# Optimization experiments

Hardware: AMD Instinct MI355X
Metric: run time of the kernel (lower is better)

The kernel has to match this reference:

```python
import jax, jax.numpy as jnp
import numpy as np

DIM = 192
NUM_HEADS = 6
KSZ = 7
MLP_RATIO = 4.0
LEVELS = 8
EPS = 1e-5


def layernorm(x, w, b):
    mu = jnp.mean(x, axis=-1, keepdims=True)
    var = jnp.mean(jnp.square(x - mu), axis=-1, keepdims=True)
    return (x - mu) * jax.lax.rsqrt(var + EPS) * w + b


def na2d(x, qkv_w, qkv_b, proj_w, proj_b, rpb):
    # Neighborhood attention 2D with relative position bias (NATTEN semantics:
    # window of KSZ x KSZ keys per query, clamped to stay inside the image).
    B, H, W, C = x.shape
    nh, hd = NUM_HEADS, C // NUM_HEADS
    scale = hd ** -0.5
    qkv = (x @ qkv_w.T + qkv_b).reshape(B, H, W, 3, nh, hd)
    q = qkv[..., 0, :, :] * scale  # [B,H,W,nh,hd]
    k = qkv[..., 1, :, :]
    v = qkv[..., 2, :, :]

    si = jnp.clip(jnp.arange(H) - KSZ // 2, 0, H - KSZ)
    idx_i = si[:, None] + jnp.arange(KSZ)  # [H,KSZ] row indices of each window
    sj = jnp.clip(jnp.arange(W) - KSZ // 2, 0, W - KSZ)
    idx_j = sj[:, None] + jnp.arange(KSZ)  # [W,KSZ]

    def gather_win(t):  # [B,H,W,nh,hd] -> [B,H,KSZ,W,KSZ,nh,hd]
        t = jnp.take(t, idx_i.reshape(-1), axis=1).reshape(B, H, KSZ, W, nh, hd)
        t = jnp.take(t, idx_j.reshape(-1), axis=3).reshape(B, H, KSZ, W, KSZ, nh, hd)
        return t

    kw = gather_win(k)
    vw = gather_win(v)

    # scores over the KSZ x KSZ neighborhood
    scores = jnp.einsum('bxynd,bxiyjnd->bxynij', q, kw)  # [B,H,W,nh,KSZ,KSZ]

    # relative position bias: rpb is [nh, 2K-1, 2K-1]
    rel_i = idx_i - jnp.arange(H)[:, None] + (KSZ - 1)  # [H,KSZ] in [0,2K-2]
    rel_j = idx_j - jnp.arange(W)[:, None] + (KSZ - 1)  # [W,KSZ]
    bias = rpb[:, rel_i][:, :, :, rel_j]  # [nh,H,KSZ,W,KSZ]
    scores = scores + bias.transpose(1, 3, 0, 2, 4)[None]

    attn = jax.nn.softmax(scores.reshape(B, H, W, nh, KSZ * KSZ), axis=-1)
    attn = attn.reshape(B, H, W, nh, KSZ, KSZ)
    out = jnp.einsum('bxynij,bxiyjnd->bxynd', attn, vw).reshape(B, H, W, C)
    return out @ proj_w.T + proj_b


def setup_inputs() -> dict:
    key = jax.random.key(0)
    ks = jax.random.split(key, 8)
    C = DIM
    hidden = int(C * MLP_RATIO)
    init = lambda k, shape: (jax.random.normal(k, shape, dtype=jnp.float32) * 0.02)
    return {
        'x': jax.random.normal(ks[0], (1, 128, 128, C), dtype=jnp.float32),
        'qkv_w': init(ks[1], (3 * C, C)),
        'qkv_b': jnp.zeros((3 * C,), jnp.float32),
        'proj_w': init(ks[2], (C, C)),
        'proj_b': jnp.zeros((C,), jnp.float32),
        'rpb': init(ks[3], (NUM_HEADS, 2 * KSZ - 1, 2 * KSZ - 1)),
        'ln1_w': jnp.ones((C,), jnp.float32),
        'ln1_b': jnp.zeros((C,), jnp.float32),
        'ln2_w': jnp.ones((C,), jnp.float32),
        'ln2_b': jnp.zeros((C,), jnp.float32),
        'fc1_w': init(ks[4], (hidden, C)),
        'fc1_b': jnp.zeros((hidden,), jnp.float32),
        'fc2_w': init(ks[5], (C, hidden)),
        'fc2_b': jnp.zeros((C,), jnp.float32),
        'gamma1': jnp.ones((LEVELS, C), jnp.float32),
        'gamma2': jnp.ones((LEVELS, C), jnp.float32),
        'quality': 4,
    }


def reference(x, qkv_w, qkv_b, proj_w, proj_b, rpb, ln1_w, ln1_b, ln2_w, ln2_b,
              fc1_w, fc1_b, fc2_w, fc2_b, gamma1, gamma2, quality):
    # eval-mode quality gating; quality is an integer so l = quality % 1 == 0
    s = int(quality) - 1
    g1 = jnp.abs(gamma1[s])
    g2 = jnp.abs(gamma2[s])

    shortcut = x
    h = layernorm(x, ln1_w, ln1_b)
    a = na2d(h, qkv_w, qkv_b, proj_w, proj_b, rpb)
    x = shortcut + g1 * a
    h2 = layernorm(x, ln2_w, ln2_b)
    m = jax.nn.gelu(h2 @ fc1_w.T + fc1_b, approximate=False) @ fc2_w.T + fc2_b
    x = x + g2 * m
    return x
```

## Files before the change

kernel.cpp:

```cpp
#include <hip/hip_runtime.h>
#include <hip/hip_bf16.h>
#include <math.h>

#define DIM 192
#define NHD 6
#define HD 32
#define KSZ 7
#define HID 768
#define IMH 128
#define IMW 128
#define NPIX (IMH*IMW)
#define WIN 14
#define KPAD 40

typedef __attribute__((ext_vector_type(8))) short short8;
typedef __attribute__((ext_vector_type(4))) float f32x4;

__global__ __launch_bounds__(256) void cvt_w(
    const float* __restrict__ qw, const float* __restrict__ pw,
    const float* __restrict__ f1, const float* __restrict__ f2,
    __hip_bfloat16* dq, __hip_bfloat16* dp, __hip_bfloat16* df1, __hip_bfloat16* df2)
{
    int blk = blockIdx.x, t = threadIdx.x;
    const float* s; __hip_bfloat16* d; int base;
    if (blk < 108)      { s = qw; d = dq;  base = blk * 1024; }
    else if (blk < 144) { s = pw; d = dp;  base = (blk - 108) * 1024; }
    else if (blk < 288) { s = f1; d = df1; base = (blk - 144) * 1024; }
    else                { s = f2; d = df2; base = (blk - 288) * 1024; }
    int idx = base + t * 4;
    float4 v4 = *(const float4*)(s + idx);
    union { ushort4 u; __hip_bfloat16 h[4]; } o;
    o.h[0] = __float2bfloat16(v4.x); o.h[1] = __float2bfloat16(v4.y);
    o.h[2] = __float2bfloat16(v4.z); o.h[3] = __float2bfloat16(v4.w);
    *(ushort4*)&d[idx] = o.u;
}

__device__ __forceinline__ void gl_lds16(const void* g, void* l) {
    __builtin_amdgcn_global_load_lds(
        (const __attribute__((address_space(1))) void*)g,
        (__attribute__((address_space(3))) void*)l, 16, 0, 0);
}

__device__ __forceinline__ short8 cvt8(float4 a, float4 b) {
    union { short8 v; __hip_bfloat16 h[8]; } u;
    u.h[0] = __float2bfloat16(a.x); u.h[1] = __float2bfloat16(a.y);
    u.h[2] = __float2bfloat16(a.z); u.h[3] = __float2bfloat16(a.w);
    u.h[4] = __float2bfloat16(b.x); u.h[5] = __float2bfloat16(b.y);
    u.h[6] = __float2bfloat16(b.z); u.h[7] = __float2bfloat16(b.w);
    return u.v;
}

__global__ __launch_bounds__(256, 2) void qkv_ln_gemm(
    const float* __restrict__ x, const float* __restrict__ lnw, const float* __restrict__ lnb,
    const __hip_bfloat16* __restrict__ W, const float* __restrict__ bias,
    float* __restrict__ qb, __hip_bfloat16* __restrict__ kb, __hip_bfloat16* __restrict__ vb)
{
    __shared__ __hip_bfloat16 As[32 * 192];
    __shared__ __hip_bfloat16 Ws2[2][64 * 192];
    int tid = threadIdx.x;
    int wave = tid >> 6, lane = tid & 63;
    int q = lane >> 4, col = lane & 15;
    int wm = (wave >> 1) * 16, wn = (wave & 1) * 32;
    int m0 = blockIdx.x * 32;

    auto stageW = [&](int ch, int buf) {
        #pragma unroll
        for (int i = 0; i < 6; i++) {
            int c = i * 256 + tid;
            int r = c / 24, kc = c - r * 24;
            gl_lds16(W + (size_t)(ch * 64 + r) * DIM + ((kc ^ (r & 7)) * 8),
                     (char*)&Ws2[buf][0] + (i * 256 + wave * 64) * 16);
        }
    };

    stageW(0, 0);

    {
        int row = tid >> 3, sub = tid & 7;
        const float4* xr = (const float4*)(x + (size_t)(m0 + row) * DIM + sub * 24);
        float4 xa[6];
        float s = 0.f;
        #pragma unroll
        for (int i = 0; i < 6; i++) {
            xa[i] = xr[i];
            s += xa[i].x + xa[i].y + xa[i].z + xa[i].w;
        }
        s += __shfl_xor(s, 1); s += __shfl_xor(s, 2); s += __shfl_xor(s, 4);
        float mu = s * (1.0f / DIM);
        float qs = 0.f;
        #pragma unroll
        for (int i = 0; i < 6; i++) {
            float a = xa[i].x - mu, b = xa[i].y - mu, c = xa[i].z - mu, d = xa[i].w - mu;
            qs += a * a + b * b + c * c + d * d;
        }
        qs += __shfl_xor(qs, 1); qs += __shfl_xor(qs, 2); qs += __shfl_xor(qs, 4);
        float rstd = rsqrtf(qs * (1.0f / DIM) + 1e-5f);
        const float4* wv = (const float4*)(lnw + sub * 24);
        const float4* bv = (const float4*)(lnb + sub * 24);
        #pragma unroll
        for (int j = 0; j < 3; j++) {
            float4 v0 = xa[j * 2], v1 = xa[j * 2 + 1];
            float4 w0 = wv[j * 2], w1 = wv[j * 2 + 1];
            float4 b0 = bv[j * 2], b1 = bv[j * 2 + 1];
            float4 o0, o1;
            o0.x = (v0.x - mu) * rstd * w0.x + b0.x;
            o0.y = (v0.y - mu) * rstd * w0.y + b0.y;
            o0.z = (v0.z - mu) * rstd * w0.z + b0.z;
            o0.w = (v0.w - mu) * rstd * w0.w + b0.w;
            o1.x = (v1.x - mu) * rstd * w1.x + b1.x;
            o1.y = (v1.y - mu) * rstd * w1.y + b1.y;
            o1.z = (v1.z - mu) * rstd * w1.z + b1.z;
            o1.w = (v1.w - mu) * rstd * w1.w + b1.w;
            int oct = sub * 3 + j;
            *(short8*)&As[row * 192 + ((oct ^ (row & 7)) * 8)] = cvt8(o0, o1);
        }
    }
    asm volatile("s_waitcnt lgkmcnt(0)" ::: "memory");
    __builtin_amdgcn_s_barrier();

    short8 af[6];
    {
        int rA = wm + col;
        #pragma unroll
        for (int ks = 0; ks < 6; ks++)
            af[ks] = *(const short8*)&As[rA * 192 + (((ks * 4 + q) ^ (rA & 7)) * 8)];
    }

    for (int ch = 0; ch < 9; ch++) {
        if (ch < 8) {
            stageW(ch + 1, (ch + 1) & 1);
            asm volatile("s_waitcnt vmcnt(6)" ::: "memory");
        } else {
            asm volatile("s_waitcnt vmcnt(0)" ::: "memory");
        }
        __builtin_amdgcn_s_barrier();
        const __hip_bfloat16* wsb = &Ws2[ch & 1][0];
        f32x4 acc[2] = {};
        #pragma unroll
        for (int ks = 0; ks < 6; ks++) {
            #pragma unroll
            for (int ni = 0; ni < 2; ni++) {
                int rB = wn + ni * 16 + col;
                short8 bf = *(const short8*)&wsb[rB * 192 + (((ks * 4 + q) ^ (rB & 7)) * 8)];
                acc[ni] = __builtin_amdgcn_mfma_f32_16x16x32_bf16(af[ks], bf, acc[ni], 0, 0, 0);
            }
        }
        #pragma unroll
        for (int ni = 0; ni < 2; ni++) {
            int n = ch * 64 + wn + ni * 16 + col;
            float bi = bias[n];
            int h18 = n >> 5;
            int sel = h18 / 6;
            int head = h18 - sel * 6;
            #pragma unroll
            for (int r4 = 0; r4 < 4; r4++) {
                int m = m0 + wm + q * 4 + r4;
                float v = acc[ni][r4] + bi;
                size_t idx = ((size_t)head * NPIX + m) * 32 + (n & 31);
                if (sel == 0)      qb[idx] = v * 0.17677669529663687f;
                else if (sel == 1) kb[idx] = __float2bfloat16(v);
                else               vb[idx] = __float2bfloat16(v);
            }
        }
        __builtin_amdgcn_s_barrier();
    }
}

__global__ __launch_bounds__(512, 2) void tail_fused(
    const __hip_bfloat16* __restrict__ A, const __hip_bfloat16* __restrict__ Wp,
    const float* __restrict__ pb, const float* __restrict__ resid,
    const float* __restrict__ gamma1, const float* __restrict__ ln2w, const float* __restrict__ ln2b,
    const __hip_bfloat16* __restrict__ W1, const float* __restrict__ b1,
    const __hip_bfloat16* __restrict__ W2, const float* __restrict__ b2,
    const float* __restrict__ gamma2, const int* __restrict__ quality,
    float* __restrict__ outf)
{
    __shared__ __hip_bfloat16 arena[64 * 768];
    __shared__ __hip_bfloat16 Wsb[2][64 * 192];
    __shared__ float lnred[2][64][2];
    __hip_bfloat16* Bsp = arena;
    __hip_bfloat16* Hs  = arena + 192 * 192;

    int tid = threadIdx.x;
    int wave = tid >> 6, lane = tid & 63;
    int q = lane >> 4, col = lane & 15;
    int wm = (wave >> 1) * 16, wh = wave & 1;
    int m0 = blockIdx.x * 64;

    const __hip_bfloat16* Ab = A + (size_t)m0 * DIM;
    #pragma unroll
    for (int i = 0; i < 3; i++) {
        int c = i * 512 + tid;
        int r = c / 24, kc = c - r * 24;
        gl_lds16(Ab + r * DIM + (kc ^ (r & 7)) * 8, (char*)Hs + (i * 512 + wave * 64) * 16);
    }
    #pragma unroll
    for (int i = 0; i < 9; i++) {
        int c = i * 512 + tid;
        int r = c / 24, kc = c - r * 24;
        gl_lds16(Wp + (size_t)r * DIM + (kc ^ (r & 7)) * 8, (char*)Bsp + (i * 512 + wave * 64) * 16);
    }
    __syncthreads();

    f32x4 acc[6] = {};
    #pragma unroll
    for (int ks = 0; ks < 6; ks++) {
        int rA = wm + col;
        short8 af = *(const short8*)&Hs[rA * DIM + (((ks * 4 + q) ^ (rA & 7)) * 8)];
        #pragma unroll
        for (int f = 0; f < 6; f++) {
            int rB = wh * 96 + f * 16 + col;
            short8 bf = *(const short8*)&Bsp[rB * DIM + (((ks * 4 + q) ^ (rB & 7)) * 8)];
            acc[f] = __builtin_amdgcn_mfma_f32_16x16x32_bf16(af, bf, acc[f], 0, 0, 0);
        }
    }

    int s = quality[0] - 1;
    float v[6][4];
    float sm[4] = {}, sq[4] = {};
    #pragma unroll
    for (int f = 0; f < 6; f++) {
        int n = wh * 96 + f * 16 + col;
        float bi = pb[n];
        float g = fabsf(gamma1[s * DIM + n]);
        #pragma unroll
        for (int r = 0; r < 4; r++) {
            int m = m0 + wm + q * 4 + r;
            v[f][r] = resid[(size_t)m * DIM + n] + g * (acc[f][r] + bi);
            sm[r] += v[f][r]; sq[r] += v[f][r] * v[f][r];
        }
    }
    #pragma unroll
    for (int off = 1; off <= 8; off <<= 1)
        #pragma unroll
        for (int r = 0; r < 4; r++) {
            sm[r] += __shfl_xor(sm[r], off);
            sq[r] += __shfl_xor(sq[r], off);
        }
    if (col == 0) {
        #pragma unroll
        for (int r = 0; r < 4; r++) {
            lnred[wh][wm + q * 4 + r][0] = sm[r];
            lnred[wh][wm + q * 4 + r][1] = sq[r];
        }
    }
    __syncthreads();
    float mu[4], rstd[4];
    #pragma unroll
    for (int r = 0; r < 4; r++) {
        int ml = wm + q * 4 + r;
        float smt = lnred[0][ml][0] + lnred[1][ml][0];
        float sqt = lnred[0][ml][1] + lnred[1][ml][1];
        mu[r] = smt * (1.0f / DIM);
        float var = sqt * (1.0f / DIM) - mu[r] * mu[r];
        rstd[r] = rsqrtf(var + 1e-5f);
    }
    #pragma unroll
    for (int f = 0; f < 6; f++) {
        int n = wh * 96 + f * 16 + col;
        float lw = ln2w[n], lb = ln2b[n];
        #pragma unroll
        for (int r = 0; r < 4; r++) {
            int ml = wm + q * 4 + r;
            Hs[ml * DIM + (((n >> 3) ^ (ml & 7)) * 8) + (n & 7)] =
                __float2bfloat16((v[f][r] - mu[r]) * rstd[r] * lw + lb);
        }
    }
    __syncthreads();
    short8 af1[6];
    {
        int rowA = wm + col;
        #pragma unroll
        for (int ks = 0; ks < 6; ks++)
            af1[ks] = *(const short8*)&Hs[rowA * DIM + (((ks * 4 + q) ^ (rowA & 7)) * 8)];
    }
    __syncthreads();

    auto stage1 = [&](int t, int buf) {
        #pragma unroll
        for (int i = 0; i < 3; i++) {
            int c = i * 512 + tid;
            int r = c / 24, kc = c - r * 24;
            gl_lds16(W1 + (size_t)(t * 64 + r) * DIM + (kc ^ (r & 7)) * 8,
                     (char*)&Wsb[buf][0] + (i * 512 + wave * 64) * 16);
        }
    };
    auto stage2 = [&](int ch, int buf) {
        #pragma unroll
        for (int i = 0; i < 3; i++) {
            int idx = i * 512 + tid;
            int r = idx >> 3, o = idx & 7;
            gl_lds16(W2 + (size_t)r * HID + ch * 64 + ((o ^ (r & 7)) * 8),
                     (char*)&Wsb[buf][0] + (i * 512 + wave * 64) * 16);
        }
    };
    __hip_bfloat16* Ms = arena;

    stage1(0, 0);
    for (int t = 0; t < 12; t++) {
        if (t < 11) stage1(t + 1, (t + 1) & 1);
        else        stage2(0, 0);
        asm volatile("s_waitcnt vmcnt(3)" ::: "memory");
        __builtin_amdgcn_s_barrier();
        const __hip_bfloat16* wsb = &Wsb[t & 1][0];
        f32x4 a1[2] = {};
        #pragma unroll
        for (int ks = 0; ks < 6; ks++) {
            #pragma unroll
            for (int ni = 0; ni < 2; ni++) {
                int r = wh * 32 + ni * 16 + col;
                short8 bf = *(const short8*)&wsb[r * DIM + (((ks * 4 + q) ^ (r & 7)) * 8)];
                a1[ni] = __builtin_amdgcn_mfma_f32_16x16x32_bf16(af1[ks], bf, a1[ni], 0, 0, 0);
            }
        }
        #pragma unroll
        for (int ni = 0; ni < 2; ni++) {
            int n = t * 64 + wh * 32 + ni * 16 + col;
            float bi = b1[n];
            int oct = n >> 3;
            #pragma unroll
            for (int r4 = 0; r4 < 4; r4++) {
                int row = wm + q * 4 + r4;
                float vv = a1[ni][r4] + bi;
                float u = 0.7978845608f * (vv + 0.044715f * vv * vv * vv);
                float tt = 1.f - 2.f / (__expf(2.f * u) + 1.f);
                vv = 0.5f * vv * (1.f + tt);
                int osw = (oct & ~7) | ((oct ^ row) & 7);
                *(__hip_bfloat16*)((char*)Ms + row * 1536 + osw * 16 + (n & 7) * 2) =
                    __float2bfloat16(vv);
            }
        }
        __builtin_amdgcn_s_barrier();
    }
    __syncthreads();

    int wn2 = wh * 96;
    f32x4 acc2[6] = {};
    for (int ch = 0; ch < 12; ch++) {
        stage2(ch < 11 ? ch + 1 : 11, (ch + 1) & 1);
        asm volatile("s_waitcnt vmcnt(3)" ::: "memory");
        __builtin_amdgcn_s_barrier();
        const __hip_bfloat16* wsb = &Wsb[ch & 1][0];
        #pragma unroll
        for (int ks = 0; ks < 2; ks++) {
            int row = wm + col;
            int og = ch * 8 + ks * 4 + q;
            int osw = (og & ~7) | ((og ^ row) & 7);
            short8 a2 = *(const short8*)((char*)Ms + row * 1536 + osw * 16);
            #pragma unroll
            for (int f = 0; f < 6; f++) {
                int r = wn2 + f * 16 + col;
                short8 bf = *(const short8*)&wsb[r * 64 + (((ks * 4 + q) ^ (r & 7)) * 8)];
                acc2[f] = __builtin_amdgcn_mfma_f32_16x16x32_bf16(a2, bf, acc2[f], 0, 0, 0);
            }
        }
        __builtin_amdgcn_s_barrier();
    }
    #pragma unroll
    for (int f = 0; f < 6; f++) {
        int n = wn2 + f * 16 + col;
        float g = fabsf(gamma2[s * DIM + n]);
        float bi = b2[n];
        #pragma unroll
        for (int r4 = 0; r4 < 4; r4++) {
            int m = m0 + wm + q * 4 + r4;
            outf[(size_t)m * DIM + n] = v[f][r4] + g * (acc2[f][r4] + bi);
        }
    }
}

__device__ __forceinline__ void unpack8(const __hip_bfloat16* ptr, float* f) {
    short8 s8 = *(const short8*)ptr;
    union { short8 v; unsigned u[4]; } c; c.v = s8;
    #pragma unroll
    for (int w = 0; w < 4; w++) {
        f[2*w]   = __uint_as_float(c.u[w] << 16);
        f[2*w+1] = __uint_as_float(c.u[w] & 0xffff0000u);
    }
}

__global__ __launch_bounds__(256, 4) void attn_kernel3(
    const float* __restrict__ qbuf, const __hip_bfloat16* __restrict__ kbuf,
    const __hip_bfloat16* __restrict__ vbuf, const float* __restrict__ rpb,
    __hip_bfloat16* __restrict__ out)
{
    __shared__ __hip_bfloat16 Ks[WIN * WIN * KPAD];
    __shared__ __hip_bfloat16 Vs[WIN * WIN * KPAD];
    __shared__ float rpbs[169];

    int head = blockIdx.y;
    int tile = blockIdx.x;
    int ti0 = (tile >> 4) * 8;
    int tj0 = (tile & 15) * 8;
    int wi0 = ti0 - 3; wi0 = wi0 < 0 ? 0 : (wi0 > IMH - WIN ? IMH - WIN : wi0);
    int wj0 = tj0 - 3; wj0 = wj0 < 0 ? 0 : (wj0 > IMW - WIN ? IMW - WIN : wj0);

    int tid = threadIdx.x;
    const size_t hbase = (size_t)head * NPIX;

    for (int c = tid; c < 784; c += 256) {
        int i = c / 56, part = c - i * 56;
        int n = i * WIN + (part >> 2);
        int dp = part & 3;
        size_t goff = (hbase + (size_t)(wi0 + i) * IMW + wj0) * 32 + part * 8;
        short8 kk = *(const short8*)(kbuf + goff);
        short8 vv = *(const short8*)(vbuf + goff);
        *(short8*)&Ks[n * KPAD + dp * 8] = kk;
        *(short8*)&Vs[n * KPAD + dp * 8] = vv;
    }
    if (tid < 169) rpbs[tid] = rpb[head * 169 + tid];

    int p   = tid >> 2;
    int sub = tid & 3;
    int pi = ti0 + (p >> 3), pj = tj0 + (p & 7);
    int si = pi - 3; si = si < 0 ? 0 : (si > IMH - KSZ ? IMH - KSZ : si);
    int sj = pj - 3; sj = sj < 0 ? 0 : (sj > IMW - KSZ ? IMW - KSZ : sj);
    int bi = si - wi0, bj = sj - wj0;

    const float4* qp = (const float4*)(qbuf + (hbase + (size_t)(pi * IMW + pj)) * 32 + sub * 8);
    float4 q0 = qp[0], q1 = qp[1];
    float q[8] = {q0.x, q0.y, q0.z, q0.w, q1.x, q1.y, q1.z, q1.w};

    __syncthreads();

    float m = -1e30f, l = 0.f;
    float acc[8] = {};
    #pragma unroll
    for (int ki = 0; ki < KSZ; ki++) {
        int rbase = (bi + ki) * WIN + bj;
        const float* rb = &rpbs[(si + ki - pi + 6) * 13 + (sj - pj + 6)];
        float s7[KSZ];
        #pragma unroll
        for (int kj = 0; kj < KSZ; kj++) {
            float kf[8];
            unpack8(&Ks[(rbase + kj) * KPAD + sub * 8], kf);
            float d = q[0]*kf[0] + q[1]*kf[1] + q[2]*kf[2] + q[3]*kf[3]
                    + q[4]*kf[4] + q[5]*kf[5] + q[6]*kf[6] + q[7]*kf[7];
            d += __shfl_xor(d, 1);
            d += __shfl_xor(d, 2);
            s7[kj] = d + rb[kj];
        }
        float rmax = s7[0];
        #pragma unroll
        for (int kj = 1; kj < KSZ; kj++) rmax = fmaxf(rmax, s7[kj]);
        float mn = fmaxf(m, rmax);
        float co = __expf(m - mn);
        l *= co;
        #pragma unroll
        for (int e = 0; e < 8; e++) acc[e] *= co;
        #pragma unroll
        for (int kj = 0; kj < KSZ; kj++) {
            float pw = __expf(s7[kj] - mn);
            l += pw;
            float vf[8];
            unpack8(&Vs[(rbase + kj) * KPAD + sub * 8], vf);
            #pragma unroll
            for (int e = 0; e < 8; e++) acc[e] += pw * vf[e];
        }
        m = mn;
    }
    float rl = 1.f / l;
    __hip_bfloat16* op = out + (size_t)(pi * IMW + pj) * DIM + head * HD + sub * 8;
    #pragma unroll
    for (int e = 0; e < 8; e++) op[e] = __float2bfloat16(acc[e] * rl);
}

extern "C" void kernel_launch(void* const* d_in, const int* in_sizes, int n_in,
                              void* d_out, int out_size, void* d_ws, size_t ws_size,
                              hipStream_t stream)
{
    const float* x      = (const float*)d_in[0];
    const float* qkv_w  = (const float*)d_in[1];
    const float* qkv_b  = (const float*)d_in[2];
    const float* proj_w = (const float*)d_in[3];
    const float* proj_b = (const float*)d_in[4];
    const float* rpb    = (const float*)d_in[5];
    const float* ln1_w  = (const float*)d_in[6];
    const float* ln1_b  = (const float*)d_in[7];
    const float* ln2_w  = (const float*)d_in[8];
    const float* ln2_b  = (const float*)d_in[9];
    const float* fc1_w  = (const float*)d_in[10];
    const float* fc1_b  = (const float*)d_in[11];
    const float* fc2_w  = (const float*)d_in[12];
    const float* fc2_b  = (const float*)d_in[13];
    const float* gamma1 = (const float*)d_in[14];
    const float* gamma2 = (const float*)d_in[15];
    const int*   quality= (const int*)d_in[16];
    float* out = (float*)d_out;

    char* ws = (char*)d_ws;
    float*          qbuf   = (float*)ws;
    __hip_bfloat16* kbuf   = (__hip_bfloat16*)(ws + 12582912);
    __hip_bfloat16* vbuf   = (__hip_bfloat16*)(ws + 18874368);
    __hip_bfloat16* attn_b = (__hip_bfloat16*)(ws + 44040192);
    __hip_bfloat16* wq     = (__hip_bfloat16*)(ws + 50331648);
    __hip_bfloat16* wp     = (__hip_bfloat16*)(ws + 50552832);
    __hip_bfloat16* wf1    = (__hip_bfloat16*)(ws + 50626560);
    __hip_bfloat16* wf2    = (__hip_bfloat16*)(ws + 50921472);

    cvt_w<<<432, 256, 0, stream>>>(qkv_w, proj_w, fc1_w, fc2_w, wq, wp, wf1, wf2);
    qkv_ln_gemm<<<512, 256, 0, stream>>>(
        x, ln1_w, ln1_b, wq, qkv_b, qbuf, kbuf, vbuf);
    attn_kernel3<<<dim3(256, NHD), 256, 0, stream>>>(qbuf, kbuf, vbuf, rpb, attn_b);
    tail_fused<<<256, 512, 0, stream>>>(
        attn_b, wp, proj_b, x, gamma1, ln2_w, ln2_b,
        wf1, fc1_b, wf2, fc2_b, gamma2, quality, out);
}
```

Before: 170.7 us.

## Widen tail kernel to 16 waves and stream proj weights through double buffer

The fused projection+MLP tail kernel now runs 1024 threads (16 waves), with each wave owning a 16-column slice. The projection weights are streamed in 64-row chunks through the existing double buffer instead of being staged whole into the arena, and W1 staging is pipelined with those chunks. Conversion of the proj/fc1/fc2 weights is moved out of the first cvt kernel into extra blocks of the attention launch, so the qkv GEMM can start sooner. This trades more waves per block, and so more register pressure and barrier cost, for better latency hiding. The extra blocks on the attention grid also add wasted early-exiting blocks for the y>0 heads.

```diff
diff --git a/kernel.cpp b/kernel.cpp
--- a/kernel.cpp
+++ b/kernel.cpp
@@ -16,23 +16,20 @@
 typedef __attribute__((ext_vector_type(8))) short short8;
 typedef __attribute__((ext_vector_type(4))) float f32x4;
 
+#define LDS_SYNC() do { \
+    asm volatile("s_waitcnt lgkmcnt(0)" ::: "memory"); \
+    __builtin_amdgcn_sched_barrier(0); \
+    __builtin_amdgcn_s_barrier(); } while (0)
+
 __global__ __launch_bounds__(256) void cvt_w(
-    const float* __restrict__ qw, const float* __restrict__ pw,
-    const float* __restrict__ f1, const float* __restrict__ f2,
-    __hip_bfloat16* dq, __hip_bfloat16* dp, __hip_bfloat16* df1, __hip_bfloat16* df2)
+    const float* __restrict__ qw, __hip_bfloat16* __restrict__ dq)
 {
-    int blk = blockIdx.x, t = threadIdx.x;
-    const float* s; __hip_bfloat16* d; int base;
-    if (blk < 108)      { s = qw; d = dq;  base = blk * 1024; }
-    else if (blk < 144) { s = pw; d = dp;  base = (blk - 108) * 1024; }
-    else if (blk < 288) { s = f1; d = df1; base = (blk - 144) * 1024; }
-    else                { s = f2; d = df2; base = (blk - 288) * 1024; }
-    int idx = base + t * 4;
-    float4 v4 = *(const float4*)(s + idx);
+    int idx = blockIdx.x * 1024 + threadIdx.x * 4;
+    float4 v4 = *(const float4*)(qw + idx);
     union { ushort4 u; __hip_bfloat16 h[4]; } o;
     o.h[0] = __float2bfloat16(v4.x); o.h[1] = __float2bfloat16(v4.y);
     o.h[2] = __float2bfloat16(v4.z); o.h[3] = __float2bfloat16(v4.w);
-    *(ushort4*)&d[idx] = o.u;
+    *(ushort4*)&dq[idx] = o.u;
 }
 
 __device__ __forceinline__ void gl_lds16(const void* g, void* l) {
@@ -48,6 +45,27 @@
     u.h[4] = __float2bfloat16(b.x); u.h[5] = __float2bfloat16(b.y);
     u.h[6] = __float2bfloat16(b.z); u.h[7] = __float2bfloat16(b.w);
     return u.v;
+}
+
+__device__ __forceinline__ void stage_rows(const __hip_bfloat16* __restrict__ src,
+                                           char* ldsbase, int wave, int lane) {
+    int c0 = wave * 96 + lane;
+    int r0 = c0 / 24, k0 = c0 - r0 * 24;
+    gl_lds16(src + (size_t)r0 * DIM + ((k0 ^ (r0 & 7)) * 8), ldsbase + (wave * 96) * 16);
+    int c1 = wave * 96 + 64 + (lane & 31);
+    int r1 = c1 / 24, k1 = c1 - r1 * 24;
+    if (lane < 32)
+        gl_lds16(src + (size_t)r1 * DIM + ((k1 ^ (r1 & 7)) * 8), ldsbase + (wave * 96 + 64) * 16);
+}
+__device__ __forceinline__ void stage_w2(const __hip_bfloat16* __restrict__ W2, int ch,
+                                         char* ldsbase, int wave, int lane) {
+    int i0 = wave * 96 + lane;
+    int r0 = i0 >> 3, o0 = i0 & 7;
+    gl_lds16(W2 + (size_t)r0 * HID + ch * 64 + ((o0 ^ (r0 & 7)) * 8), ldsbase + (wave * 96) * 16);
+    int i1 = wave * 96 + 64 + (lane & 31);
+    int r1 = i1 >> 3, o1 = i1 & 7;
+    if (lane < 32)
+        gl_lds16(W2 + (size_t)r1 * HID + ch * 64 + ((o1 ^ (r1 & 7)) * 8), ldsbase + (wave * 96 + 64) * 16);
 }
 
 __global__ __launch_bounds__(256, 2) void qkv_ln_gemm(
@@ -116,6 +134,7 @@
         }
     }
     asm volatile("s_waitcnt lgkmcnt(0)" ::: "memory");
+    __builtin_amdgcn_sched_barrier(0);
     __builtin_amdgcn_s_barrier();
 
     short8 af[6];
@@ -166,7 +185,7 @@
     }
 }
 
-__global__ __launch_bounds__(512, 2) void tail_fused(
+__global__ __launch_bounds__(1024, 4) void tail_fused(
     const __hip_bfloat16* __restrict__ A, const __hip_bfloat16* __restrict__ Wp,
     const float* __restrict__ pb, const float* __restrict__ resid,
     const float* __restrict__ gamma1, const float* __restrict__ ln2w, const float* __restrict__ ln2b,
@@ -177,59 +196,63 @@
 {
     __shared__ __hip_bfloat16 arena[64 * 768];
     __shared__ __hip_bfloat16 Wsb[2][64 * 192];
-    __shared__ float lnred[2][64][2];
-    __hip_bfloat16* Bsp = arena;
-    __hip_bfloat16* Hs  = arena + 192 * 192;
+    __shared__ float lnred[4][64][2];
+    __hip_bfloat16* Hs = arena + 36864;
 
     int tid = threadIdx.x;
     int wave = tid >> 6, lane = tid & 63;
     int q = lane >> 4, col = lane & 15;
-    int wm = (wave >> 1) * 16, wh = wave & 1;
+    int wm = (wave >> 2) * 16, wq4 = wave & 3;
     int m0 = blockIdx.x * 64;
-
-    const __hip_bfloat16* Ab = A + (size_t)m0 * DIM;
-    #pragma unroll
-    for (int i = 0; i < 3; i++) {
-        int c = i * 512 + tid;
-        int r = c / 24, kc = c - r * 24;
-        gl_lds16(Ab + r * DIM + (kc ^ (r & 7)) * 8, (char*)Hs + (i * 512 + wave * 64) * 16);
-    }
-    #pragma unroll
-    for (int i = 0; i < 9; i++) {
-        int c = i * 512 + tid;
-        int r = c / 24, kc = c - r * 24;
-        gl_lds16(Wp + (size_t)r * DIM + (kc ^ (r & 7)) * 8, (char*)Bsp + (i * 512 + wave * 64) * 16);
-    }
-    __syncthreads();
-
-    f32x4 acc[6] = {};
-    #pragma unroll
-    for (int ks = 0; ks < 6; ks++) {
+    int s = quality[0] - 1;
+
+    stage_rows(A + (size_t)m0 * DIM, (char*)Hs, wave, lane);
+    stage_rows(Wp, (char*)&Wsb[0][0], wave, lane);
+    stage_rows(Wp + 64 * DIM, (char*)&Wsb[1][0], wave, lane);
+    asm volatile("s_waitcnt vmcnt(2)" ::: "memory");
+    __builtin_amdgcn_s_barrier();
+
+    short8 afp[6];
+    {
         int rA = wm + col;
-        short8 af = *(const short8*)&Hs[rA * DIM + (((ks * 4 + q) ^ (rA & 7)) * 8)];
-        #pragma unroll
-        for (int f = 0; f < 6; f++) {
-            int rB = wh * 96 + f * 16 + col;
-            short8 bf = *(const short8*)&Bsp[rB * DIM + (((ks * 4 + q) ^ (rB & 7)) * 8)];
-            acc[f] = __builtin_amdgcn_mfma_f32_16x16x32_bf16(af, bf, acc[f], 0, 0, 0);
-        }
-    }
-
-    int s = quality[0] - 1;
-    float v[6][4];
+        #pragma unroll
+        for (int ks = 0; ks < 6; ks++)
+            afp[ks] = *(const short8*)&Hs[rA * 192 + (((ks * 4 + q) ^ (rA & 7)) * 8)];
+    }
+
+    float v[3][4];
     float sm[4] = {}, sq[4] = {};
-    #pragma unroll
-    for (int f = 0; f < 6; f++) {
-        int n = wh * 96 + f * 16 + col;
+    auto proj_chunk = [&](int ch, const __hip_bfloat16* wsb) {
+        f32x4 pacc = {};
+        int rB = wq4 * 16 + col;
+        #pragma unroll
+        for (int ks = 0; ks < 6; ks++) {
+            short8 bf = *(const short8*)&wsb[rB * 192 + (((ks * 4 + q) ^ (rB & 7)) * 8)];
+            pacc = __builtin_amdgcn_mfma_f32_16x16x32_bf16(afp[ks], bf, pacc, 0, 0, 0);
+        }
+        int n = ch * 64 + wq4 * 16 + col;
         float bi = pb[n];
         float g = fabsf(gamma1[s * DIM + n]);
         #pragma unroll
         for (int r = 0; r < 4; r++) {
             int m = m0 + wm + q * 4 + r;
-            v[f][r] = resid[(size_t)m * DIM + n] + g * (acc[f][r] + bi);
-            sm[r] += v[f][r]; sq[r] += v[f][r] * v[f][r];
-        }
-    }
+            v[ch][r] = resid[(size_t)m * DIM + n] + g * (pacc[r] + bi);
+            sm[r] += v[ch][r]; sq[r] += v[ch][r] * v[ch][r];
+        }
+    };
+
+    proj_chunk(0, &Wsb[0][0]);
+    __builtin_amdgcn_s_barrier();
+    stage_rows(Wp + 128 * DIM, (char*)&Wsb[0][0], wave, lane);
+    asm volatile("s_waitcnt vmcnt(2)" ::: "memory");
+    __builtin_amdgcn_s_barrier();
+    proj_chunk(1, &Wsb[1][0]);
+    __builtin_amdgcn_s_barrier();
+    stage_rows(W1, (char*)&Wsb[1][0], wave, lane);
+    asm volatile("s_waitcnt vmcnt(2)" ::: "memory");
+    __builtin_amdgcn_s_barrier();
+    proj_chunk(2, &Wsb[0][0]);
+
     #pragma unroll
     for (int off = 1; off <= 8; off <<= 1)
         #pragma unroll
@@ -240,125 +263,102 @@
     if (col == 0) {
         #pragma unroll
         for (int r = 0; r < 4; r++) {
-            lnred[wh][wm + q * 4 + r][0] = sm[r];
-            lnred[wh][wm + q * 4 + r][1] = sq[r];
-        }
-    }
-    __syncthreads();
+            lnred[wq4][wm + q * 4 + r][0] = sm[r];
+            lnred[wq4][wm + q * 4 + r][1] = sq[r];
+        }
+    }
+    LDS_SYNC();
     float mu[4], rstd[4];
     #pragma unroll
     for (int r = 0; r < 4; r++) {
         int ml = wm + q * 4 + r;
-        float smt = lnred[0][ml][0] + lnred[1][ml][0];
-        float sqt = lnred[0][ml][1] + lnred[1][ml][1];
+        float smt = lnred[0][ml][0] + lnred[1][ml][0] + lnred[2][ml][0] + lnred[3][ml][0];
+        float sqt = lnred[0][ml][1] + lnred[1][ml][1] + lnred[2][ml][1] + lnred[3][ml][1];
         mu[r] = smt * (1.0f / DIM);
         float var = sqt * (1.0f / DIM) - mu[r] * mu[r];
         rstd[r] = rsqrtf(var + 1e-5f);
     }
     #pragma unroll
-    for (int f = 0; f < 6; f++) {
-        int n = wh * 96 + f * 16 + col;
+    for (int ch = 0; ch < 3; ch++) {
+        int n = ch * 64 + wq4 * 16 + col;
         float lw = ln2w[n], lb = ln2b[n];
         #pragma unroll
         for (int r = 0; r < 4; r++) {
             int ml = wm + q * 4 + r;
-            Hs[ml * DIM + (((n >> 3) ^ (ml & 7)) * 8) + (n & 7)] =
-                __float2bfloat16((v[f][r] - mu[r]) * rstd[r] * lw + lb);
-        }
-    }
-    __syncthreads();
+            Hs[ml * 192 + (((n >> 3) ^ (ml & 7)) * 8) + (n & 7)] =
+                __float2bfloat16((v[ch][r] - mu[r]) * rstd[r] * lw + lb);
+        }
+    }
+    LDS_SYNC();
     short8 af1[6];
     {
         int rowA = wm + col;
         #pragma unroll
         for (int ks = 0; ks < 6; ks++)
-            af1[ks] = *(const short8*)&Hs[rowA * DIM + (((ks * 4 + q) ^ (rowA & 7)) * 8)];
-    }
-    __syncthreads();
-
-    auto stage1 = [&](int t, int buf) {
-        #pragma unroll
-        for (int i = 0; i < 3; i++) {
-            int c = i * 512 + tid;
-            int r = c / 24, kc = c - r * 24;
-            gl_lds16(W1 + (size_t)(t * 64 + r) * DIM + (kc ^ (r & 7)) * 8,
-                     (char*)&Wsb[buf][0] + (i * 512 + wave * 64) * 16);
-        }
-    };
-    auto stage2 = [&](int ch, int buf) {
-        #pragma unroll
-        for (int i = 0; i < 3; i++) {
-            int idx = i * 512 + tid;
-            int r = idx >> 3, o = idx & 7;
-            gl_lds16(W2 + (size_t)r * HID + ch * 64 + ((o ^ (r & 7)) * 8),
-                     (char*)&Wsb[buf][0] + (i * 512 + wave * 64) * 16);
-        }
-    };
-    __hip_bfloat16* Ms = arena;
-
-    stage1(0, 0);
+            af1[ks] = *(const short8*)&Hs[rowA * 192 + (((ks * 4 + q) ^ (rowA & 7)) * 8)];
+    }
+    LDS_SYNC();
+
     for (int t = 0; t < 12; t++) {
-        if (t < 11) stage1(t + 1, (t + 1) & 1);
-        else        stage2(0, 0);
-        asm volatile("s_waitcnt vmcnt(3)" ::: "memory");
+        if (t < 11) stage_rows(W1 + (size_t)(t + 1) * 64 * DIM, (char*)&Wsb[t & 1][0], wave, lane);
+        else        stage_w2(W2, 0, (char*)&Wsb[1][0], wave, lane);
+        asm volatile("s_waitcnt vmcnt(2)" ::: "memory");
         __builtin_amdgcn_s_barrier();
-        const __hip_bfloat16* wsb = &Wsb[t & 1][0];
-        f32x4 a1[2] = {};
+        const __hip_bfloat16* wsb = &Wsb[(t + 1) & 1][0];
+        f32x4 a1 = {};
+        int rB = wq4 * 16 + col;
         #pragma unroll
         for (int ks = 0; ks < 6; ks++) {
-            #pragma unroll
-            for (int ni = 0; ni < 2; ni++) {
-                int r = wh * 32 + ni * 16 + col;
-                short8 bf = *(const short8*)&wsb[r * DIM + (((ks * 4 + q) ^ (r & 7)) * 8)];
-                a1[ni] = __builtin_amdgcn_mfma_f32_16x16x32_bf16(af1[ks], bf, a1[ni], 0, 0, 0);
-            }
-        }
-        #pragma unroll
-        for (int ni = 0; ni < 2; ni++) {
-            int n = t * 64 + wh * 32 + ni * 16 + col;
-            float bi = b1[n];
-            int oct = n >> 3;
-            #pragma unroll
-            for (int r4 = 0; r4 < 4; r4++) {
-                int row = wm + q * 4 + r4;
-                float vv = a1[ni][r4] + bi;
-                float u = 0.7978845608f * (vv + 0.044715f * vv * vv * vv);
-                float tt = 1.f - 2.f / (__expf(2.f * u) + 1.f);
-                vv = 0.5f * vv * (1.f + tt);
-                int osw = (oct & ~7) | ((oct ^ row) & 7);
-                *(__hip_bfloat16*)((char*)Ms + row * 1536 + osw * 16 + (n & 7) * 2) =
-                    __float2bfloat16(vv);
-            }
+            short8 bf = *(const short8*)&wsb[rB * 192 + (((ks * 4 + q) ^ (rB & 7)) * 8)];
+            a1 = __builtin_amdgcn_mfma_f32_16x16x32_bf16(af1[ks], bf, a1, 0, 0, 0);
+        }
+        int n = t * 64 + wq4 * 16 + col;
+        float bi = b1[n];
+        int oct = n >> 3;
+        #pragma unroll
+        for (int r4 = 0; r4 < 4; r4++) {
+            int row = wm + q * 4 + r4;
+            float vv = a1[r4] + bi;
+            float u = 0.7978845608f * (vv + 0.044715f * vv * vv * vv);
+            float tt = 1.f - 2.f / (__expf(2.f * u) + 1.f);
+            vv = 0.5f * vv * (1.f + tt);
+            int osw = (oct & ~7) | ((oct ^ row) & 7);
+            *(__hip_bfloat16*)((char*)arena + row * 1536 + osw * 16 + (n & 7) * 2) =
+                __float2bfloat16(vv);
         }
         __builtin_amdgcn_s_barrier();
     }
-    __syncthreads();
-
-    int wn2 = wh * 96;
-    f32x4 acc2[6] = {};
+    LDS_SYNC();
+
+    f32x4 acc2[3] = {};
     for (int ch = 0; ch < 12; ch++) {
-        stage2(ch < 11 ? ch + 1 : 11, (ch + 1) & 1);
-        asm volatile("s_waitcnt vmcnt(3)" ::: "memory");
+        if (ch < 11) {
+            stage_w2(W2, ch + 1, (char*)&Wsb[ch & 1][0], wave, lane);
+            asm volatile("s_waitcnt vmcnt(2)" ::: "memory");
+        } else {
+            asm volatile("s_waitcnt vmcnt(0)" ::: "memory");
+        }
         __builtin_amdgcn_s_barrier();
-        const __hip_bfloat16* wsb = &Wsb[ch & 1][0];
+        const __hip_bfloat16* wsb = &Wsb[(ch + 1) & 1][0];
         #pragma unroll
         for (int ks = 0; ks < 2; ks++) {
             int row = wm + col;
             int og = ch * 8 + ks * 4 + q;
             int osw = (og & ~7) | ((og ^ row) & 7);
-            short8 a2 = *(const short8*)((char*)Ms + row * 1536 + osw * 16);
+            short8 a2 = *(const short8*)((char*)arena + row * 1536 + osw * 16);
             #pragma unroll
-            for (int f = 0; f < 6; f++) {
-                int r = wn2 + f * 16 + col;
-                short8 bf = *(const short8*)&wsb[r * 64 + (((ks * 4 + q) ^ (r & 7)) * 8)];
+            for (int f = 0; f < 3; f++) {
+                int rB = f * 64 + wq4 * 16 + col;
+                short8 bf = *(const short8*)&wsb[rB * 64 + (((ks * 4 + q) ^ (rB & 7)) * 8)];
                 acc2[f] = __builtin_amdgcn_mfma_f32_16x16x32_bf16(a2, bf, acc2[f], 0, 0, 0);
             }
         }
         __builtin_amdgcn_s_barrier();
     }
-    #pragma unroll
-    for (int f = 0; f < 6; f++) {
-        int n = wn2 + f * 16 + col;
+
+    #pragma unroll
+    for (int f = 0; f < 3; f++) {
+        int n = f * 64 + wq4 * 16 + col;
         float g = fabsf(gamma2[s * DIM + n]);
         float bi = b2[n];
         #pragma unroll
@@ -382,8 +382,26 @@
 __global__ __launch_bounds__(256, 4) void attn_kernel3(
     const float* __restrict__ qbuf, const __hip_bfloat16* __restrict__ kbuf,
     const __hip_bfloat16* __restrict__ vbuf, const float* __restrict__ rpb,
-    __hip_bfloat16* __restrict__ out)
+    __hip_bfloat16* __restrict__ out,
+    const float* __restrict__ pw, const float* __restrict__ f1w, const float* __restrict__ f2w,
+    __hip_bfloat16* __restrict__ dp, __hip_bfloat16* __restrict__ df1, __hip_bfloat16* __restrict__ df2)
 {
+    if (blockIdx.x >= 256) {
+        if (blockIdx.y != 0) return;
+        int blk = blockIdx.x - 256, t = threadIdx.x;
+        const float* s; __hip_bfloat16* d; int base;
+        if (blk < 36)       { s = pw;  d = dp;  base = blk * 1024; }
+        else if (blk < 180) { s = f1w; d = df1; base = (blk - 36) * 1024; }
+        else                { s = f2w; d = df2; base = (blk - 180) * 1024; }
+        int idx = base + t * 4;
+        float4 v4 = *(const float4*)(s + idx);
+        union { ushort4 u; __hip_bfloat16 h[4]; } o;
+        o.h[0] = __float2bfloat16(v4.x); o.h[1] = __float2bfloat16(v4.y);
+        o.h[2] = __float2bfloat16(v4.z); o.h[3] = __float2bfloat16(v4.w);
+        *(ushort4*)&d[idx] = o.u;
+        return;
+    }
+
     __shared__ __hip_bfloat16 Ks[WIN * WIN * KPAD];
     __shared__ __hip_bfloat16 Vs[WIN * WIN * KPAD];
     __shared__ float rpbs[169];
@@ -401,12 +419,12 @@
     for (int c = tid; c < 784; c += 256) {
         int i = c / 56, part = c - i * 56;
         int n = i * WIN + (part >> 2);
-        int dp = part & 3;
+        int dp2 = part & 3;
         size_t goff = (hbase + (size_t)(wi0 + i) * IMW + wj0) * 32 + part * 8;
         short8 kk = *(const short8*)(kbuf + goff);
         short8 vv = *(const short8*)(vbuf + goff);
-        *(short8*)&Ks[n * KPAD + dp * 8] = kk;
-        *(short8*)&Vs[n * KPAD + dp * 8] = vv;
+        *(short8*)&Ks[n * KPAD + dp2 * 8] = kk;
+        *(short8*)&Vs[n * KPAD + dp2 * 8] = vv;
     }
     if (tid < 169) rpbs[tid] = rpb[head * 169 + tid];
 
@@ -450,12 +468,12 @@
         for (int e = 0; e < 8; e++) acc[e] *= co;
         #pragma unroll
         for (int kj = 0; kj < KSZ; kj++) {
-            float pw = __expf(s7[kj] - mn);
-            l += pw;
+            float pw2 = __expf(s7[kj] - mn);
+            l += pw2;
             float vf[8];
             unpack8(&Vs[(rbase + kj) * KPAD + sub * 8], vf);
             #pragma unroll
-            for (int e = 0; e < 8; e++) acc[e] += pw * vf[e];
+            for (int e = 0; e < 8; e++) acc[e] += pw2 * vf[e];
         }
         m = mn;
     }
@@ -498,11 +516,12 @@
     __hip_bfloat16* wf1    = (__hip_bfloat16*)(ws + 50626560);
     __hip_bfloat16* wf2    = (__hip_bfloat16*)(ws + 50921472);
 
-    cvt_w<<<432, 256, 0, stream>>>(qkv_w, proj_w, fc1_w, fc2_w, wq, wp, wf1, wf2);
+    cvt_w<<<108, 256, 0, stream>>>(qkv_w, wq);
     qkv_ln_gemm<<<512, 256, 0, stream>>>(
         x, ln1_w, ln1_b, wq, qkv_b, qbuf, kbuf, vbuf);
-    attn_kernel3<<<dim3(256, NHD), 256, 0, stream>>>(qbuf, kbuf, vbuf, rpb, attn_b);
-    tail_fused<<<256, 512, 0, stream>>>(
+    attn_kernel3<<<dim3(256 + 324, NHD), 256, 0, stream>>>(
+        qbuf, kbuf, vbuf, rpb, attn_b, proj_w, fc1_w, fc2_w, wp, wf1, wf2);
+    tail_fused<<<256, 1024, 0, stream>>>(
         attn_b, wp, proj_b, x, gamma1, ln2_w, ln2_b,
         wf1, fc1_b, wf2, fc2_b, gamma2, quality, out);
 }
```

Result: no change. 170.5 us (-0.1%).
